# Kernel tuning notes

Measured on AMD Instinct MI355X. Metric: run time of the kernel, lower is better.

The kernel has to match this reference:

```python
import jax, jax.numpy as jnp
import numpy as np

HIDDEN = 2048
N_HEADS = 16
HEAD_DIM = HIDDEN // N_HEADS
SEQ = 4096
ROPE_BASE = 10000.0


def setup_inputs() -> dict:
    key = jax.random.key(0)
    ks = jax.random.split(key, 5)
    sc = 1.0 / np.sqrt(HIDDEN)
    return {
        "hidden_states": jax.random.normal(ks[0], (SEQ, HIDDEN), jnp.float32),
        "Wq": jax.random.normal(ks[1], (HIDDEN, HIDDEN), jnp.float32) * sc,
        "Wk": jax.random.normal(ks[2], (HIDDEN, HIDDEN), jnp.float32) * sc,
        "Wv": jax.random.normal(ks[3], (HIDDEN, HIDDEN), jnp.float32) * sc,
        "Wo": jax.random.normal(ks[4], (HIDDEN, HIDDEN), jnp.float32) * sc,
    }


def _rope_cos_sin(seq_len, head_dim, dtype):
    # Llama-style rotary embedding tables, shape [S, 1, head_dim]
    inv_freq = 1.0 / (ROPE_BASE ** (jnp.arange(0, head_dim, 2, dtype=jnp.float32) / head_dim))
    pos = jnp.arange(seq_len, dtype=jnp.float32)
    freqs = pos[:, None] * inv_freq[None, :]          # [S, d/2]
    emb = jnp.concatenate([freqs, freqs], axis=-1)     # [S, d]
    return jnp.cos(emb)[:, None, :].astype(dtype), jnp.sin(emb)[:, None, :].astype(dtype)


def _rotate_half(x):
    h = x.shape[-1] // 2
    return jnp.concatenate([-x[..., h:], x[..., :h]], axis=-1)


def reference(hidden_states, Wq, Wk, Wv, Wo):
    S, H = hidden_states.shape
    d = HEAD_DIM
    # QKV projections (nn.Linear: x @ W.T), split into heads: [S, nH, d]
    q = (hidden_states @ Wq.T).reshape(S, N_HEADS, d)
    k = (hidden_states @ Wk.T).reshape(S, N_HEADS, d)
    v = (hidden_states @ Wv.T).reshape(S, N_HEADS, d)
    # Per-position RoPE on q and k
    cos, sin = _rope_cos_sin(S, d, q.dtype)
    q = q * cos + _rotate_half(q) * sin
    k = k * cos + _rotate_half(k) * sin
    # Causal scaled-dot-product attention, scores [nH, S, S]
    scores = jnp.einsum("snd,tnd->nst", q, k) / jnp.sqrt(jnp.asarray(d, q.dtype))
    causal = jnp.tril(jnp.ones((S, S), dtype=bool))
    scores = jnp.where(causal[None, :, :], scores, jnp.asarray(-1e30, scores.dtype))
    probs = jax.nn.softmax(scores, axis=-1)
    ctx = jnp.einsum("nst,tnd->snd", probs, v).reshape(S, H)
    return ctx @ Wo.T
```

## Files before the change

kernel.cpp:

```cpp
#include <hip/hip_runtime.h>

#define SEQ 4096
#define HIDDEN 2048
#define NHEADS 16
#define HDIM 128
#define QBLK 128
#define KVB 64

typedef float f32x4 __attribute__((ext_vector_type(4)));
typedef __bf16 bf16x8 __attribute__((ext_vector_type(8)));
typedef unsigned int u32x4 __attribute__((ext_vector_type(4)));
typedef unsigned short u16x8 __attribute__((ext_vector_type(8)));
typedef unsigned short u16;

#define SCL2 0.12751747456918851f
#define RLOG 0.2076205059304601f

__device__ __forceinline__ u16 f2bf(float f) {
  unsigned u = __float_as_uint(f);
  unsigned r = 0x7fffu + ((u >> 16) & 1u);
  return (u16)((u + r) >> 16);
}
__device__ __forceinline__ float bf2f(u16 u) {
  return __uint_as_float(((unsigned)u) << 16);
}
__device__ __forceinline__ unsigned cvtpk(float a, float b) {
  unsigned r;
  asm volatile("v_cvt_pk_bf16_f32 %0, %1, %2" : "=v"(r) : "v"(a), "v"(b));
  return r;
}

__device__ __forceinline__ void gload16(const u16* g, u16* l) {
  __builtin_amdgcn_global_load_lds(
      (const __attribute__((address_space(1))) unsigned int*)g,
      (__attribute__((address_space(3))) unsigned int*)l, 16, 0, 0);
}

__device__ __forceinline__ int cumq(int q) {
  return q < 24 ? (q - 12) * 2 : 24 + (q - 24) * 3;
}

__global__ __launch_bounds__(256) void cvt5(const float* __restrict__ X,
    const float* __restrict__ Wq, const float* __restrict__ Wk,
    const float* __restrict__ Wv, const float* __restrict__ Wo,
    u16* __restrict__ dst) {
  const size_t SH = (size_t)SEQ * HIDDEN, HH = (size_t)HIDDEN * HIDDEN;
  size_t i = ((size_t)blockIdx.x * 256 + threadIdx.x) * 8;
  const float* src; size_t off;
  if (i < SH) { src = X; off = i; }
  else if (i < SH + HH) { src = Wq; off = i - SH; }
  else if (i < SH + 2 * HH) { src = Wk; off = i - SH - HH; }
  else if (i < SH + 3 * HH) { src = Wv; off = i - SH - 2 * HH; }
  else { src = Wo; off = i - SH - 3 * HH; }
  float4 a = *reinterpret_cast<const float4*>(src + off);
  float4 b = *reinterpret_cast<const float4*>(src + off + 4);
  u16x8 o;
  o[0] = f2bf(a.x); o[1] = f2bf(a.y); o[2] = f2bf(a.z); o[3] = f2bf(a.w);
  o[4] = f2bf(b.x); o[5] = f2bf(b.y); o[6] = f2bf(b.z); o[7] = f2bf(b.w);
  *reinterpret_cast<u32x4*>(dst + i) = __builtin_bit_cast(u32x4, o);
}

__global__ __launch_bounds__(256, 3) void gemm_qkv(const u16* __restrict__ Xb,
    const u16* __restrict__ Wqb, const u16* __restrict__ Wkb,
    const u16* __restrict__ Wvb, u16* __restrict__ Qo, u16* __restrict__ Ko,
    u16* __restrict__ Vt) {
  __shared__ u16 As[3][4096];
  __shared__ u16 Bs[3][4096];
  const int wg = blockIdx.x;
  const int swz = (wg & 7) * 192 + (wg >> 3);
  const int z = swz >> 9;
  const int rr_ = swz & 511;
  const u16 *A, *B;
  u16* C;
  int bm, bn, cst;
  if (z == 2) {
    A = Wvb; B = Xb; C = Vt;
    bm = (rr_ & 15) << 7; bn = (rr_ >> 4) << 7; cst = SEQ;
  } else {
    A = Xb; B = z ? Wkb : Wqb; C = z ? Ko : Qo;
    bm = (rr_ & 31) << 7; bn = (rr_ >> 5) << 7; cst = HIDDEN;
  }
  const int t = threadIdx.x, lane = t & 63, wave = t >> 6;
  const int lrow = lane & 15, lk = (lane >> 4) * 8;
  const int wr = wave * 32;
  const int r0 = t >> 2, c0 = (t & 3) * 8;

  f32x4 acc[2][8] = {};

  const u16* Ab = A + (size_t)(bm + r0) * HIDDEN + c0;
  const u16* Bb = B + (size_t)(bn + r0) * HIDDEN + c0;
  const size_t rstep = (size_t)64 * HIDDEN;

#define QKV_STAGE(tt, s)                                            \
  {                                                                 \
    const int ko = (tt) * 32;                                       \
    gload16(Ab + ko, &As[s][t * 8]);                                \
    gload16(Bb + ko, &Bs[s][t * 8]);                                \
    gload16(Ab + rstep + ko, &As[s][2048 + t * 8]);                 \
    gload16(Bb + rstep + ko, &Bs[s][2048 + t * 8]);                 \
  }

  QKV_STAGE(0, 0);
  QKV_STAGE(1, 1);
  asm volatile("s_waitcnt vmcnt(4)" ::: "memory");
  __builtin_amdgcn_s_barrier();
  asm volatile("" ::: "memory");

  int sa = 0, sb = 1, sc = 2;
  for (int tt = 0; tt < 64; ++tt) {
    if (tt + 2 < 64) QKV_STAGE(tt + 2, sc);
    bf16x8 af[2], bfv[8];
#pragma unroll
    for (int m = 0; m < 2; ++m)
      af[m] = __builtin_bit_cast(bf16x8,
          *reinterpret_cast<const u32x4*>(&As[sa][(wr + m * 16 + lrow) * 32 + lk]));
#pragma unroll
    for (int n = 0; n < 8; ++n)
      bfv[n] = __builtin_bit_cast(bf16x8,
          *reinterpret_cast<const u32x4*>(&Bs[sa][(n * 16 + lrow) * 32 + lk]));
#pragma unroll
    for (int n = 0; n < 8; ++n)
#pragma unroll
      for (int m = 0; m < 2; ++m)
        acc[m][n] = __builtin_amdgcn_mfma_f32_16x16x32_bf16(af[m], bfv[n], acc[m][n], 0, 0, 0);
    asm volatile("s_waitcnt vmcnt(4)" ::: "memory");
    __builtin_amdgcn_sched_barrier(0);
    __builtin_amdgcn_s_barrier();
    asm volatile("" ::: "memory");
    int s_ = sa; sa = sb; sb = sc; sc = s_;
  }
#undef QKV_STAGE

  const int rb = (lane >> 4) * 4;
  if (z < 2) {
    const float qscale = (z == 0) ? SCL2 : 1.0f;
#pragma unroll
    for (int m = 0; m < 2; ++m)
#pragma unroll
      for (int q = 0; q < 4; ++q) {
        const int s = bm + wr + m * 16 + rb + q;
#pragma unroll
        for (int n = 0; n < 4; ++n) {
          const int ii = n * 16 + lrow;
          float inv = exp2f((float)ii * -RLOG);
          float ang = (float)s * inv;
          float sn, cs;
          __sincosf(ang, &sn, &cs);
          sn *= qscale; cs *= qscale;
          float x1 = acc[m][n][q], x2 = acc[m][n + 4][q];
          acc[m][n][q] = x1 * cs - x2 * sn;
          acc[m][n + 4][q] = x2 * cs + x1 * sn;
        }
      }
  }
#pragma unroll
  for (int m = 0; m < 2; ++m)
#pragma unroll
    for (int n = 0; n < 8; ++n)
#pragma unroll
      for (int q = 0; q < 4; ++q) {
        int col;
        if (z == 2)
          col = bn + (n >> 2) * 64 + ((n >> 1) & 1) * 32 + (lrow >> 2) * 8 +
                (n & 1) * 4 + (lrow & 3);
        else
          col = bn + n * 16 + lrow;
        C[(size_t)(bm + wr + m * 16 + rb + q) * cst + col] = f2bf(acc[m][n][q]);
      }
}

__global__ __launch_bounds__(256, 3) void gemm_out(const u16* __restrict__ A,
    const u16* __restrict__ B, float* __restrict__ C) {
  __shared__ u16 As[2][128 * 32];
  __shared__ u16 Bs[2][128 * 32];
  const int wg = blockIdx.x;
  const int swz = (wg & 7) * 64 + (wg >> 3);
  const int bm = (swz & 31) << 7;
  const int bn = (swz >> 5) << 7;
  const int t = threadIdx.x, lane = t & 63, wave = t >> 6;
  const int lrow = lane & 15, lk = (lane >> 4) * 8;
  const int wr = wave * 32;
  const int r0 = t >> 2, c0 = (t & 3) * 8;

  f32x4 acc[2][8] = {};

#pragma unroll
  for (int is = 0; is < 2; ++is) {
    gload16(A + (size_t)(bm + is * 64 + r0) * HIDDEN + c0, &As[0][is * 2048 + t * 8]);
    gload16(B + (size_t)(bn + is * 64 + r0) * HIDDEN + c0, &Bs[0][is * 2048 + t * 8]);
  }
  __syncthreads();

  int p = 0;
  for (int kt = 0; kt < HIDDEN; kt += 32) {
    if (kt + 32 < HIDDEN) {
#pragma unroll
      for (int is = 0; is < 2; ++is) {
        gload16(A + (size_t)(bm + is * 64 + r0) * HIDDEN + kt + 32 + c0,
                &As[p ^ 1][is * 2048 + t * 8]);
        gload16(B + (size_t)(bn + is * 64 + r0) * HIDDEN + kt + 32 + c0,
                &Bs[p ^ 1][is * 2048 + t * 8]);
      }
    }
    bf16x8 af[2], bfv[8];
#pragma unroll
    for (int m = 0; m < 2; ++m)
      af[m] = __builtin_bit_cast(bf16x8,
          *reinterpret_cast<const u32x4*>(&As[p][(wr + m * 16 + lrow) * 32 + lk]));
#pragma unroll
    for (int n = 0; n < 8; ++n)
      bfv[n] = __builtin_bit_cast(bf16x8,
          *reinterpret_cast<const u32x4*>(&Bs[p][(n * 16 + lrow) * 32 + lk]));
#pragma unroll
    for (int n = 0; n < 8; ++n)
#pragma unroll
      for (int m = 0; m < 2; ++m)
        acc[m][n] = __builtin_amdgcn_mfma_f32_16x16x32_bf16(af[m], bfv[n], acc[m][n], 0, 0, 0);
    __syncthreads();
    p ^= 1;
  }

  const int rb = (lane >> 4) * 4;
#pragma unroll
  for (int m = 0; m < 2; ++m)
#pragma unroll
    for (int n = 0; n < 8; ++n)
#pragma unroll
      for (int q = 0; q < 4; ++q)
        C[(size_t)(bm + wr + m * 16 + rb + q) * HIDDEN + bn + n * 16 + lrow] =
            acc[m][n][q];
}

__global__ __launch_bounds__(512, 4) void attn_kernel(const u16* __restrict__ Q,
                                                      const u16* __restrict__ Kg,
                                                      const u16* __restrict__ Vt,
                                                      u16* __restrict__ O,
                                                      u16* __restrict__ Opart,
                                                      float* __restrict__ Ml) {
  __shared__ u16 Ks[2][KVB * 128];
  __shared__ u16 Vs[2][128 * KVB];
  const int t = threadIdx.x;
  const int wave = t >> 6;
  const int lane = t & 63;
  const int lrow = lane & 15;
  const int lgrp = lane >> 4;

  const int g = blockIdx.x;
  const int h = g & 15;
  const int e = g >> 4;
  int q, c, nc;
  if (e < 24)      { q = 24 + e / 3;           c = e % 3;         nc = 3; }
  else if (e < 48) { q = 23 - ((e - 24) >> 1); c = (e - 24) & 1;  nc = 2; }
  else             { q = 59 - e;               c = 0;             nc = 1; }
  const int total = 2 * q + 2;
  const int base = total / nc, rem = total - base * nc;
  const int it0 = c * base + (c < rem ? c : rem);
  const int it1 = it0 + base + (c < rem ? 1 : 0);

  const int qw = q * QBLK + wave * 16;

  bf16x8 qf[4];
#pragma unroll
  for (int kk = 0; kk < 4; ++kk)
    qf[kk] = __builtin_bit_cast(bf16x8, *reinterpret_cast<const u32x4*>(
        Q + (size_t)(qw + lrow) * HIDDEN + h * HDIM + kk * 32 + lgrp * 8));

  const u16* kgb[2]; const u16* vgb[2]; int kof[2], vof[2];
#pragma unroll
  for (int is = 0; is < 2; ++is) {
    int ch = is * 512 + t;
    int krow = ch >> 4, kslot = ch & 15;
    int kcol = ((kslot & 8) | ((kslot ^ krow) & 7)) * 8;
    kgb[is] = Kg + (size_t)krow * HIDDEN + h * HDIM + kcol;
    kof[is] = ch * 8;
    int vrow = ch >> 3, vslot = ch & 7;
    int vcol = ((vslot ^ vrow) & 7) * 8;
    vgb[is] = Vt + (size_t)(h * HDIM + vrow) * SEQ + vcol;
    vof[is] = ch * 8;
  }

  f32x4 acc[8] = {};
  float m2 = -1e30f;
  float lsum = 0.f;

#pragma unroll
  for (int is = 0; is < 2; ++is) {
    gload16(kgb[is] + (size_t)(it0 * KVB) * HIDDEN, &Ks[0][kof[is]]);
    gload16(vgb[is] + it0 * KVB, &Vs[0][vof[is]]);
  }
  __syncthreads();

  int p = 0;
  for (int bt = it0; bt < it1; ++bt) {
    const int t0 = bt * KVB;
    if (bt + 1 < it1) {
      const int t1 = (bt + 1) * KVB;
#pragma unroll
      for (int is = 0; is < 2; ++is) {
        gload16(kgb[is] + (size_t)t1 * HIDDEN, &Ks[p ^ 1][kof[is]]);
        gload16(vgb[is] + t1, &Vs[p ^ 1][vof[is]]);
      }
    }

    if (t0 <= qw + 15) {
      const bool need_mask = (t0 + KVB - 1 > qw);
      f32x4 sc[4] = {};
      __builtin_amdgcn_s_setprio(1);
#pragma unroll
      for (int kk = 0; kk < 4; ++kk) {
#pragma unroll
        for (int colf = 0; colf < 4; ++colf) {
          int trow = colf * 16 + lrow;
          int slot = kk * 4 + lgrp;
          bf16x8 kf = __builtin_bit_cast(bf16x8, *reinterpret_cast<const u32x4*>(
              &Ks[p][trow * 128 + ((slot & 8) | ((slot ^ trow) & 7)) * 8]));
          sc[colf] = __builtin_amdgcn_mfma_f32_16x16x32_bf16(kf, qf[kk], sc[colf], 0, 0, 0);
        }
      }
      __builtin_amdgcn_s_setprio(0);

      const int qg = qw + lrow;
      float mx = -3.0e38f;
#pragma unroll
      for (int colf = 0; colf < 4; ++colf) {
        const int kvb0 = t0 + colf * 16 + lgrp * 4;
#pragma unroll
        for (int r = 0; r < 4; ++r) {
          float v = sc[colf][r];
          if (need_mask) v = (kvb0 + r <= qg) ? v : -1e30f;
          sc[colf][r] = v;
          mx = fmaxf(mx, v);
        }
      }
      mx = fmaxf(mx, __shfl_xor(mx, 16));
      mx = fmaxf(mx, __shfl_xor(mx, 32));

      if (__any(mx > m2 + 11.5f)) {
        float mn = fmaxf(m2, mx);
        float sf = exp2f(m2 - mn);
        m2 = mn;
        lsum *= sf;
#pragma unroll
        for (int r = 0; r < 4; ++r) {
          float sfr = __shfl(sf, (lane & 48) | (lgrp * 4 + r));
#pragma unroll
          for (int nn = 0; nn < 8; ++nn) acc[nn][r] *= sfr;
        }
      }

      unsigned paw[2][4];
      float ps = 0.f;
#pragma unroll
      for (int colf = 0; colf < 4; ++colf) {
        float pv[4];
#pragma unroll
        for (int r = 0; r < 4; ++r) {
          pv[r] = exp2f(sc[colf][r] - m2);
          ps += pv[r];
        }
        paw[colf >> 1][(colf & 1) * 2 + 0] = cvtpk(pv[0], pv[1]);
        paw[colf >> 1][(colf & 1) * 2 + 1] = cvtpk(pv[2], pv[3]);
      }
      ps += __shfl_xor(ps, 16);
      ps += __shfl_xor(ps, 32);
      lsum += ps;

      __builtin_amdgcn_s_setprio(1);
#pragma unroll
      for (int ks = 0; ks < 2; ++ks) {
        u32x4 w = {paw[ks][0], paw[ks][1], paw[ks][2], paw[ks][3]};
        bf16x8 pa = __builtin_bit_cast(bf16x8, w);
#pragma unroll
        for (int nn = 0; nn < 8; ++nn) {
          const int d = nn * 16 + lrow;
          bf16x8 vb = __builtin_bit_cast(bf16x8, *reinterpret_cast<const u32x4*>(
              &Vs[p][d * 64 + (((ks * 4 + lgrp) ^ d) & 7) * 8]));
          acc[nn] = __builtin_amdgcn_mfma_f32_16x16x32_bf16(pa, vb, acc[nn], 0, 0, 0);
        }
      }
      __builtin_amdgcn_s_setprio(0);
    }

    __syncthreads();
    p ^= 1;
  }

  if (nc == 1) {
    float inv[4];
#pragma unroll
    for (int r = 0; r < 4; ++r) {
      float lsr = __shfl(lsum, (lane & 48) | (lgrp * 4 + r));
      inv[r] = 1.0f / lsr;
    }
#pragma unroll
    for (int nn = 0; nn < 8; ++nn)
#pragma unroll
      for (int r = 0; r < 4; ++r) {
        int row = qw + lgrp * 4 + r;
        int col = h * HDIM + nn * 16 + lrow;
        O[(size_t)row * HIDDEN + col] = f2bf(acc[nn][r] * inv[r]);
      }
  } else {
    const int slot = h * 48 + cumq(q) + c;
    u16* Op = Opart + (size_t)slot * (QBLK * HDIM);
    float* ml = Ml + (size_t)slot * 256;
#pragma unroll
    for (int nn = 0; nn < 8; ++nn)
#pragma unroll
      for (int r = 0; r < 4; ++r) {
        int rl = wave * 16 + lgrp * 4 + r;
        Op[rl * HDIM + nn * 16 + lrow] = f2bf(acc[nn][r]);
      }
    if (lgrp == 0) {
      int rl = wave * 16 + lrow;
      ml[rl] = m2;
      ml[128 + rl] = lsum;
    }
  }
}

__global__ __launch_bounds__(256) void combine_kernel(const u16* __restrict__ Opart,
                                                      const float* __restrict__ Ml,
                                                      u16* __restrict__ O) {
  const int bid = blockIdx.x;
  const int h = bid / 20;
  const int q = 12 + bid % 20;
  const int nc = (q < 24) ? 2 : 3;
  const int sbase = h * 48 + cumq(q);
  const int r = threadIdx.x >> 1;
  const int d0 = (threadIdx.x & 1) * 64;

  float w[3], l = 0.f, M = -3.0e38f;
#pragma unroll
  for (int c = 0; c < 3; ++c)
    if (c < nc) M = fmaxf(M, Ml[(size_t)(sbase + c) * 256 + r]);
#pragma unroll
  for (int c = 0; c < 3; ++c)
    if (c < nc) {
      w[c] = exp2f(Ml[(size_t)(sbase + c) * 256 + r] - M);
      l += w[c] * Ml[(size_t)(sbase + c) * 256 + 128 + r];
    }
  const float inv = 1.0f / l;

  for (int dd = 0; dd < 64; dd += 8) {
    float a8[8] = {};
#pragma unroll
    for (int c = 0; c < 3; ++c)
      if (c < nc) {
        u16x8 v = *reinterpret_cast<const u16x8*>(
            Opart + (size_t)(sbase + c) * (QBLK * HDIM) + r * HDIM + d0 + dd);
#pragma unroll
        for (int j = 0; j < 8; ++j) a8[j] += w[c] * bf2f(v[j]);
      }
    u16x8 o8;
#pragma unroll
    for (int j = 0; j < 8; ++j) o8[j] = f2bf(a8[j] * inv);
    *reinterpret_cast<u16x8*>(
        &O[(size_t)(q * QBLK + r) * HIDDEN + h * HDIM + d0 + dd]) = o8;
  }
}

extern "C" void kernel_launch(void* const* d_in, const int* in_sizes, int n_in,
                              void* d_out, int out_size, void* d_ws, size_t ws_size,
                              hipStream_t stream) {
  const float* X  = (const float*)d_in[0];
  const float* Wq = (const float*)d_in[1];
  const float* Wk = (const float*)d_in[2];
  const float* Wv = (const float*)d_in[3];
  const float* Wo = (const float*)d_in[4];
  float* out = (float*)d_out;

  u16* ws = (u16*)d_ws;
  const size_t SH = (size_t)SEQ * HIDDEN;
  const size_t HH = (size_t)HIDDEN * HIDDEN;
  u16* Xb  = ws;
  u16* Wqb = Xb + SH;
  u16* Wkb = Wqb + HH;
  u16* Wvb = Wkb + HH;
  u16* Wob = Wvb + HH;
  u16* Qb  = Wob + HH;
  u16* Kb  = Qb + SH;
  u16* Vtb = Kb + SH;
  u16* Cb  = Vtb + SH;

  u16* Opart = ws;
  float* Ml = (float*)(ws + (size_t)768 * 16384);

  cvt5<<<(int)((SH + 4 * HH) / 2048), 256, 0, stream>>>(X, Wq, Wk, Wv, Wo, ws);

  gemm_qkv<<<1536, 256, 0, stream>>>(Xb, Wqb, Wkb, Wvb, Qb, Kb, Vtb);

  attn_kernel<<<960, 512, 0, stream>>>(Qb, Kb, Vtb, Cb, Opart, Ml);
  combine_kernel<<<320, 256, 0, stream>>>(Opart, Ml, Cb);

  gemm_out<<<512, 256, 0, stream>>>(Cb, Wob, out);
}
```

Before: 335.2 us.

## Triple-buffer output GEMM and compute softmax row sums via MFMA ones

```diff
diff --git a/kernel.cpp b/kernel.cpp
--- a/kernel.cpp
+++ b/kernel.cpp
@@ -171,8 +171,8 @@
 
 __global__ __launch_bounds__(256, 3) void gemm_out(const u16* __restrict__ A,
     const u16* __restrict__ B, float* __restrict__ C) {
-  __shared__ u16 As[2][128 * 32];
-  __shared__ u16 Bs[2][128 * 32];
+  __shared__ u16 As[3][4096];
+  __shared__ u16 Bs[3][4096];
   const int wg = blockIdx.x;
   const int swz = (wg & 7) * 64 + (wg >> 3);
   const int bm = (swz & 31) << 7;
@@ -184,41 +184,49 @@
 
   f32x4 acc[2][8] = {};
 
-#pragma unroll
-  for (int is = 0; is < 2; ++is) {
-    gload16(A + (size_t)(bm + is * 64 + r0) * HIDDEN + c0, &As[0][is * 2048 + t * 8]);
-    gload16(B + (size_t)(bn + is * 64 + r0) * HIDDEN + c0, &Bs[0][is * 2048 + t * 8]);
-  }
-  __syncthreads();
-
-  int p = 0;
-  for (int kt = 0; kt < HIDDEN; kt += 32) {
-    if (kt + 32 < HIDDEN) {
-#pragma unroll
-      for (int is = 0; is < 2; ++is) {
-        gload16(A + (size_t)(bm + is * 64 + r0) * HIDDEN + kt + 32 + c0,
-                &As[p ^ 1][is * 2048 + t * 8]);
-        gload16(B + (size_t)(bn + is * 64 + r0) * HIDDEN + kt + 32 + c0,
-                &Bs[p ^ 1][is * 2048 + t * 8]);
-      }
-    }
+  const u16* Ab = A + (size_t)(bm + r0) * HIDDEN + c0;
+  const u16* Bb = B + (size_t)(bn + r0) * HIDDEN + c0;
+  const size_t rstep = (size_t)64 * HIDDEN;
+
+#define OUT_STAGE(tt, s)                                            \
+  {                                                                 \
+    const int ko = (tt) * 32;                                       \
+    gload16(Ab + ko, &As[s][t * 8]);                                \
+    gload16(Bb + ko, &Bs[s][t * 8]);                                \
+    gload16(Ab + rstep + ko, &As[s][2048 + t * 8]);                 \
+    gload16(Bb + rstep + ko, &Bs[s][2048 + t * 8]);                 \
+  }
+
+  OUT_STAGE(0, 0);
+  OUT_STAGE(1, 1);
+  asm volatile("s_waitcnt vmcnt(4)" ::: "memory");
+  __builtin_amdgcn_s_barrier();
+  asm volatile("" ::: "memory");
+
+  int sa = 0, sb = 1, sc = 2;
+  for (int tt = 0; tt < 64; ++tt) {
+    if (tt + 2 < 64) OUT_STAGE(tt + 2, sc);
     bf16x8 af[2], bfv[8];
 #pragma unroll
     for (int m = 0; m < 2; ++m)
       af[m] = __builtin_bit_cast(bf16x8,
-          *reinterpret_cast<const u32x4*>(&As[p][(wr + m * 16 + lrow) * 32 + lk]));
+          *reinterpret_cast<const u32x4*>(&As[sa][(wr + m * 16 + lrow) * 32 + lk]));
 #pragma unroll
     for (int n = 0; n < 8; ++n)
       bfv[n] = __builtin_bit_cast(bf16x8,
-          *reinterpret_cast<const u32x4*>(&Bs[p][(n * 16 + lrow) * 32 + lk]));
+          *reinterpret_cast<const u32x4*>(&Bs[sa][(n * 16 + lrow) * 32 + lk]));
 #pragma unroll
     for (int n = 0; n < 8; ++n)
 #pragma unroll
       for (int m = 0; m < 2; ++m)
         acc[m][n] = __builtin_amdgcn_mfma_f32_16x16x32_bf16(af[m], bfv[n], acc[m][n], 0, 0, 0);
-    __syncthreads();
-    p ^= 1;
-  }
+    asm volatile("s_waitcnt vmcnt(4)" ::: "memory");
+    __builtin_amdgcn_sched_barrier(0);
+    __builtin_amdgcn_s_barrier();
+    asm volatile("" ::: "memory");
+    int s_ = sa; sa = sb; sb = sc; sc = s_;
+  }
+#undef OUT_STAGE
 
   const int rb = (lane >> 4) * 4;
 #pragma unroll
@@ -265,6 +273,11 @@
     qf[kk] = __builtin_bit_cast(bf16x8, *reinterpret_cast<const u32x4*>(
         Q + (size_t)(qw + lrow) * HIDDEN + h * HDIM + kk * 32 + lgrp * 8));
 
+  u16x8 ow;
+#pragma unroll
+  for (int j = 0; j < 8; ++j) ow[j] = (lrow == 0) ? 0x3F80 : 0;
+  const bf16x8 vones = __builtin_bit_cast(bf16x8, ow);
+
   const u16* kgb[2]; const u16* vgb[2]; int kof[2], vof[2];
 #pragma unroll
   for (int is = 0; is < 2; ++is) {
@@ -280,8 +293,8 @@
   }
 
   f32x4 acc[8] = {};
+  f32x4 acc1 = {};
   float m2 = -1e30f;
-  float lsum = 0.f;
 
 #pragma unroll
   for (int is = 0; is < 2; ++is) {
@@ -320,18 +333,21 @@
       __builtin_amdgcn_s_setprio(0);
 
       const int qg = qw + lrow;
-      float mx = -3.0e38f;
-#pragma unroll
-      for (int colf = 0; colf < 4; ++colf) {
-        const int kvb0 = t0 + colf * 16 + lgrp * 4;
-#pragma unroll
-        for (int r = 0; r < 4; ++r) {
-          float v = sc[colf][r];
-          if (need_mask) v = (kvb0 + r <= qg) ? v : -1e30f;
-          sc[colf][r] = v;
-          mx = fmaxf(mx, v);
+      if (need_mask) {
+#pragma unroll
+        for (int colf = 0; colf < 4; ++colf) {
+          const int kvb0 = t0 + colf * 16 + lgrp * 4;
+#pragma unroll
+          for (int r = 0; r < 4; ++r)
+            sc[colf][r] = (kvb0 + r <= qg) ? sc[colf][r] : -1e30f;
         }
       }
+      float mc[4];
+#pragma unroll
+      for (int colf = 0; colf < 4; ++colf)
+        mc[colf] = fmaxf(fmaxf(sc[colf][0], sc[colf][1]),
+                         fmaxf(sc[colf][2], sc[colf][3]));
+      float mx = fmaxf(fmaxf(mc[0], mc[1]), fmaxf(mc[2], mc[3]));
       mx = fmaxf(mx, __shfl_xor(mx, 16));
       mx = fmaxf(mx, __shfl_xor(mx, 32));
 
@@ -339,31 +355,24 @@
         float mn = fmaxf(m2, mx);
         float sf = exp2f(m2 - mn);
         m2 = mn;
-        lsum *= sf;
 #pragma unroll
         for (int r = 0; r < 4; ++r) {
           float sfr = __shfl(sf, (lane & 48) | (lgrp * 4 + r));
 #pragma unroll
           for (int nn = 0; nn < 8; ++nn) acc[nn][r] *= sfr;
+          acc1[r] *= sfr;
         }
       }
 
       unsigned paw[2][4];
-      float ps = 0.f;
 #pragma unroll
       for (int colf = 0; colf < 4; ++colf) {
         float pv[4];
 #pragma unroll
-        for (int r = 0; r < 4; ++r) {
-          pv[r] = exp2f(sc[colf][r] - m2);
-          ps += pv[r];
-        }
+        for (int r = 0; r < 4; ++r) pv[r] = exp2f(sc[colf][r] - m2);
         paw[colf >> 1][(colf & 1) * 2 + 0] = cvtpk(pv[0], pv[1]);
         paw[colf >> 1][(colf & 1) * 2 + 1] = cvtpk(pv[2], pv[3]);
       }
-      ps += __shfl_xor(ps, 16);
-      ps += __shfl_xor(ps, 32);
-      lsum += ps;
 
       __builtin_amdgcn_s_setprio(1);
 #pragma unroll
@@ -377,6 +386,7 @@
               &Vs[p][d * 64 + (((ks * 4 + lgrp) ^ d) & 7) * 8]));
           acc[nn] = __builtin_amdgcn_mfma_f32_16x16x32_bf16(pa, vb, acc[nn], 0, 0, 0);
         }
+        acc1 = __builtin_amdgcn_mfma_f32_16x16x32_bf16(pa, vones, acc1, 0, 0, 0);
       }
       __builtin_amdgcn_s_setprio(0);
     }
@@ -388,10 +398,8 @@
   if (nc == 1) {
     float inv[4];
 #pragma unroll
-    for (int r = 0; r < 4; ++r) {
-      float lsr = __shfl(lsum, (lane & 48) | (lgrp * 4 + r));
-      inv[r] = 1.0f / lsr;
-    }
+    for (int r = 0; r < 4; ++r)
+      inv[r] = 1.0f / __shfl(acc1[r], lane & 48);
 #pragma unroll
     for (int nn = 0; nn < 8; ++nn)
 #pragma unroll
@@ -414,7 +422,11 @@
     if (lgrp == 0) {
       int rl = wave * 16 + lrow;
       ml[rl] = m2;
-      ml[128 + rl] = lsum;
+    }
+    if (lrow == 0) {
+#pragma unroll
+      for (int r = 0; r < 4; ++r)
+        ml[128 + wave * 16 + lgrp * 4 + r] = acc1[r];
     }
   }
 }
```

New measurement: 327.0 us. -2.4%, faster.
